# Kernel optimization log

Hardware: AMD Instinct MI355X
Metric: run time of the kernel (lower is better)

## Reference

```python
import jax, jax.numpy as jnp
import numpy as np

B, S, D = 128, 50, 128
NUM_NODE = 40000
HOP, N_ITER, SAMPLE = 2, 2, 12
N_NEI = 8
TEMP, MU, LEAK = 0.5, 0.1, 0.2


def setup_inputs() -> dict:
    key = jax.random.key(0)
    ks = jax.random.split(key, 32)
    stdv = 1.0 / np.sqrt(D)
    u = lambda k, shp: jax.random.uniform(k, shp, jnp.float32, -stdv, stdv)
    return {
        "inputs": jax.random.randint(ks[0], (B, S), 0, NUM_NODE),
        "adj": jax.random.randint(ks[1], (B, S, S), 0, 5),
        "item": jax.random.randint(ks[2], (B, S), 0, NUM_NODE),
        "simi_mask": jax.random.randint(ks[3], (B, S, S), 0, 2),
        "as_items_0": jax.random.randint(ks[4], (B, S, N_NEI), 0, NUM_NODE),
        "as_items_1": jax.random.randint(ks[5], (B, S, N_NEI), 0, NUM_NODE),
        "as_items_ssl_0": jax.random.randint(ks[6], (B, S, N_NEI), 0, NUM_NODE),
        "as_items_ssl_1": jax.random.randint(ks[7], (B, S, N_NEI), 0, NUM_NODE),
        "last_item_mask": jnp.zeros((B, S), bool).at[:, -1].set(True),
        "adj_all": jax.random.randint(ks[8], (NUM_NODE, SAMPLE), 0, NUM_NODE),
        "num": jax.random.uniform(ks[9], (NUM_NODE, SAMPLE)),
        "emb": u(ks[10], (NUM_NODE, D)),
        "pos_emb": u(ks[11], (200, D)),
        "a_local": u(ks[12], (N_ITER, 4, D)),
        "mir_w1": u(ks[13], (N_ITER, D, D)),
        "mir_w2": u(ks[14], (N_ITER, D, D)),
        "glob_w1": u(ks[15], (HOP, D + 1, D)),
        "glob_w2": u(ks[16], (HOP, D, 1)),
        "glob_w3": u(ks[17], (HOP, 2 * D, D)),
        "attr_w": u(ks[18], (2 * D, D)),
        "highway_w": u(ks[19], (2 * D, D)),
        "glu1_w": u(ks[20], (D, D)),
        "glu2_w": u(ks[21], (D, D)),
        "glu4_w": u(ks[22], (D, D)),
        "glu4_b": u(ks[23], (D,)),
        "w_s": u(ks[24], (D, 1)),
        "gate_w": u(ks[25], (2 * D, D)),
    }


def _forward(num, emb, pos_emb, a_local, mir_w1, mir_w2, glob_w1, glob_w2, glob_w3,
             attr_w, highway_w, glu1_w, glu2_w, glu4_w, glu4_b, w_s, gate_w,
             inputs, adj, item, simi_mask, as_lists, as_ssl_lists, last_item_mask, adj_all):
    mi = (inputs != 0).astype(emb.dtype)  # [B,S]
    h = emb[inputs]                        # [B,S,D]

    # ---- AttributeAggregator (masked-mean pool per attribute + gated fusion) ----
    def pool(idx_list):
        ps = []
        for idx in idx_list:
            m = (idx != 0).astype(emb.dtype)[..., None]  # [B,S,N,1]
            ps.append(jnp.sum(emb[idx] * m, 2) / (jnp.sum(m, 2) + 1e-8))
        return jnp.mean(jnp.stack(ps), 0)  # [B,S,D]
    hf1 = pool(as_lists)
    hf2 = pool(as_ssl_lists)
    g_attr = jax.nn.sigmoid(jnp.concatenate([h, hf1], -1) @ attr_w)
    hf = g_attr * h + (1.0 - g_attr) * hf1

    # ---- multi-hop neighbor sampling (irregular gathers) ----
    neigh = [inputs]
    wts = []
    for _ in range(HOP):
        flat = neigh[-1].reshape(-1)
        neigh.append(adj_all[flat].reshape(B, -1))
        wts.append(num[flat].reshape(B, -1))
    ev = [emb[n] for n in neigh]  # [B,S,D], [B,S*12,D], [B,S*144,D]

    item_emb = emb[item] * mi[..., None]
    sess = jnp.sum(item_emb, 1) / jnp.sum(mi, -1, keepdims=True)  # [B,D]

    # ---- GlobalAggregator stack (GCE-GNN style attention over sampled neighbors) ----
    for n_hop in range(HOP):
        nxt = []
        for hop in range(HOP - n_hop):
            sv = ev[hop]                                   # [B,M,D]
            nv = ev[hop + 1].reshape(B, -1, SAMPLE, D)     # [B,M,12,D]
            nw = wts[hop].reshape(B, -1, SAMPLE)           # [B,M,12]
            extra = jnp.broadcast_to(sess[:, None, None, :], nv.shape)
            a = jnp.concatenate([extra * nv, nw[..., None]], -1)  # [B,M,12,D+1]
            a = jax.nn.leaky_relu(a @ glob_w1[n_hop], LEAK)
            a = jax.nn.softmax((a @ glob_w2[n_hop])[..., 0], -1)[..., None]
            agg = jnp.sum(a * nv, -2)
            nxt.append(jnp.tanh(jnp.concatenate([sv, agg], -1) @ glob_w3[n_hop]))
        ev = nxt
    h_global = ev[0].reshape(B, S, D)

    # ---- LocalAggregator (edge-typed GAT) + MirrorAggregator (gated exchange) ----
    x = h
    mirror = hf
    for i in range(HOP):
        e = jax.nn.leaky_relu(jnp.einsum('bid,bjd,kd->kbij', x, x, a_local[i]), LEAK)
        att = jnp.full((B, S, S), -9e15, x.dtype)
        for k in range(4):
            att = jnp.where(adj == k + 1, e[k], att)
        x = jax.nn.softmax(att, -1) @ x
        gm = jax.nn.sigmoid(x @ mir_w1[i] + mirror @ mir_w2[i])
        x, mirror = gm * x + (1.0 - gm) * mirror, gm * mirror + (1.0 - gm) * x

    # ---- highway + last-item select ----
    g = jax.nn.sigmoid(jnp.concatenate([h, x], -1) @ highway_w)
    x_dot = g * h + (1.0 - g) * x
    h_local = jnp.sum(x_dot * last_item_mask[..., None].astype(x_dot.dtype), 1)  # [B,D]

    mask = mi[..., None]
    pos = pos_emb[:S][None]  # [1,S,D]
    bw = emb[1:]             # [NUM_NODE-1,D]
    hs = jnp.sum(h_global * mask, -2) / jnp.sum(mask, 1)  # [B,D]

    # ---- SSL pairwise similarity loss ----
    sim = jnp.einsum('bid,bjd->bij', hf1, hf2) / TEMP
    l = -jnp.log(jax.nn.softmax(sim, 2) + 1e-8)
    simi_loss = jnp.mean(jnp.sum(l * (simi_mask == 1), (1, 2)))

    # ---- attention-style GLU scoring ----
    hp = x_dot + pos
    nh = jax.nn.sigmoid(hp @ glu1_w + hs[:, None, :] @ glu2_w + h_local[:, None, :] @ glu4_w + glu4_b)
    beta = (nh @ w_s) * mask
    zg = jnp.sum(beta * hp, 1)  # [B,D]
    gf = jax.nn.sigmoid(jnp.concatenate([zg, h_local], -1) @ gate_w) * MU
    zh = gf * h_local + (1.0 - gf) * zg
    scores = zh @ bw.T  # [B, NUM_NODE-1]
    return simi_loss, scores


def reference(inputs, adj, item, simi_mask, as_items_0, as_items_1,
              as_items_ssl_0, as_items_ssl_1, last_item_mask, adj_all, num,
              emb, pos_emb, a_local, mir_w1, mir_w2, glob_w1, glob_w2, glob_w3,
              attr_w, highway_w, glu1_w, glu2_w, glu4_w, glu4_b, w_s, gate_w):
    return _forward(num, emb, pos_emb, a_local, mir_w1, mir_w2, glob_w1, glob_w2, glob_w3,
                    attr_w, highway_w, glu1_w, glu2_w, glu4_w, glu4_b, w_s, gate_w,
                    inputs, adj, item, simi_mask, [as_items_0, as_items_1],
                    [as_items_ssl_0, as_items_ssl_1], last_item_mask, adj_all)
```

## Files before the change

### kernel.cpp

```cpp
#include <hip/hip_runtime.h>
#include <hip/hip_bf16.h>
#include <type_traits>


#define B 128
#define S 50
#define D 128
#define SAMPLE 12
#define NNEI 8
#define NODES 40000
#define NSC (NODES - 1)
#define LEAK 0.2f
#define TEMPV 0.5f
#define MUV 0.1f
#define NEG_BIG -3.0e38f

typedef const float* fpp;
typedef float* fpw;
typedef unsigned short u16;
typedef __attribute__((ext_vector_type(8))) short bfrag8;
typedef __attribute__((ext_vector_type(4))) float f32x4;

__device__ __forceinline__ float sigm(float x) { return 1.f / (1.f + __expf(-x)); }
__device__ __forceinline__ float tanh_f(float x) { return 1.f - 2.f / (__expf(2.f * x) + 1.f); }
__device__ __forceinline__ float leaky(float x) { return x >= 0.f ? x : LEAK * x; }
__device__ __forceinline__ u16 f2bf(float v) {
  __hip_bfloat16 h = __float2bfloat16(v);
  return *reinterpret_cast<u16*>(&h);
}
__device__ __forceinline__ float lde(const float* p, long i) { return p[i]; }
__device__ __forceinline__ float lde(const u16* p, long i) {
  union { unsigned int u; float f; } c;
  c.u = ((unsigned int)p[i]) << 16;
  return c.f;
}
__device__ __forceinline__ float bfu(short s) {
  union { unsigned u; float f; } c;
  c.u = ((unsigned)(unsigned short)s) << 16;
  return c.f;
}

template <typename ET>
__device__ __forceinline__ bfrag8 load_frag(const ET* __restrict__ emb, long row, int koff) {
  if constexpr (sizeof(ET) == 2) {
    return *(const bfrag8*)(const void*)(emb + row * D + koff);
  } else {
    const float* s = (const float*)(emb + row * D + koff);
    float4 lo = *(const float4*)s;
    float4 hi = *(const float4*)(s + 4);
    bfrag8 b;
    b[0] = (short)f2bf(lo.x); b[1] = (short)f2bf(lo.y);
    b[2] = (short)f2bf(lo.z); b[3] = (short)f2bf(lo.w);
    b[4] = (short)f2bf(hi.x); b[5] = (short)f2bf(hi.y);
    b[6] = (short)f2bf(hi.z); b[7] = (short)f2bf(hi.w);
    return b;
  }
}

__device__ __forceinline__ bfrag8 scale8(bfrag8 r, float4 sa, float4 sb) {
  bfrag8 o;
  o[0] = (short)f2bf(bfu(r[0]) * sa.x); o[1] = (short)f2bf(bfu(r[1]) * sa.y);
  o[2] = (short)f2bf(bfu(r[2]) * sa.z); o[3] = (short)f2bf(bfu(r[3]) * sa.w);
  o[4] = (short)f2bf(bfu(r[4]) * sb.x); o[5] = (short)f2bf(bfu(r[5]) * sb.y);
  o[6] = (short)f2bf(bfu(r[6]) * sb.z); o[7] = (short)f2bf(bfu(r[7]) * sb.w);
  return o;
}

__global__ __launch_bounds__(256) void kprep_emb(fpp emb, u16* __restrict__ out) {
  long i = ((long)blockIdx.x * 256 + threadIdx.x) * 4;
  if (i + 3 >= (long)NODES * D) return;
  float4 v = *(const float4*)(emb + i);
  out[i + 0] = f2bf(v.x); out[i + 1] = f2bf(v.y);
  out[i + 2] = f2bf(v.z); out[i + 3] = f2bf(v.w);
}

__global__ __launch_bounds__(256) void kprep4(fpp gw1, fpp gw3,
                                              u16* __restrict__ p1a,
                                              u16* __restrict__ p1b,
                                              u16* __restrict__ p3a,
                                              u16* __restrict__ p3b) {
  int i = blockIdx.x * 256 + threadIdx.x;
  fpp W; u16* dst; int KS;
  if (i < 16384)      { W = gw1;             dst = p1a; KS = 4; }
  else if (i < 32768) { W = gw1 + 129 * 128; dst = p1b; KS = 4; i -= 16384; }
  else if (i < 65536) { W = gw3;             dst = p3a; KS = 8; i -= 32768; }
  else                { W = gw3 + 256 * 128; dst = p3b; KS = 8; i -= 65536; }
  int e = i & 7;
  int lane = (i >> 3) & 63;
  int rest = i >> 9;
  int ks = rest % KS, nt = rest / KS;
  int k = ks * 32 + ((lane >> 4) << 3) + e;
  int n = (nt << 4) + (lane & 15);
  dst[i] = f2bf(W[(long)k * 128 + n]);
}

template <typename ET>
__global__ __launch_bounds__(128) void k1_gather(
    const int* __restrict__ inputs, const int* __restrict__ as0,
    const int* __restrict__ as1, const int* __restrict__ ss0,
    const int* __restrict__ ss1, const ET* __restrict__ emb, fpp attr_w,
    fpw h, fpw hf1, fpw hf2, float* __restrict__ mi, fpw xA, fpw mir) {
  int bs = blockIdx.x;
  int d = threadIdx.x;
  __shared__ float h_s[D], hf1_s[D];
  int inp = inputs[bs];
  float hv = lde(emb, (long)inp * D + d);
  const int* lists[4] = {as0, as1, ss0, ss1};
  float p[4];
#pragma unroll
  for (int l = 0; l < 4; l++) {
    float sum = 0.f, cnt = 0.f;
    const int* L = lists[l] + (long)bs * NNEI;
#pragma unroll
    for (int n = 0; n < NNEI; n++) {
      int idx = L[n];
      if (idx != 0) { sum += lde(emb, (long)idx * D + d); cnt += 1.f; }
    }
    p[l] = sum / (cnt + 1e-8f);
  }
  float hf1v = 0.5f * (p[0] + p[1]);
  float hf2v = 0.5f * (p[2] + p[3]);
  h_s[d] = hv;
  hf1_s[d] = hf1v;
  __syncthreads();
  float acc = 0.f;
  for (int k = 0; k < D; k++)
    acc += h_s[k] * attr_w[(long)k * D + d] + hf1_s[k] * attr_w[(long)(D + k) * D + d];
  float g = sigm(acc);
  float hfv = g * hv + (1.f - g) * hf1v;
  long o = (long)bs * D + d;
  h[o] = hv; hf1[o] = hf1v; hf2[o] = hf2v; xA[o] = hv; mir[o] = hfv;
  if (d == 0) mi[bs] = (inp != 0) ? 1.f : 0.f;
}

__global__ __launch_bounds__(128) void k2_sess(const int* __restrict__ inputs,
                                               const int* __restrict__ item,
                                               fpp emb, fpw sess) {
  int b = blockIdx.x;
  int d = threadIdx.x;
  float acc = 0.f, ms = 0.f;
  for (int s = 0; s < S; s++) {
    int inp = inputs[b * S + s];
    float m = (inp != 0) ? 1.f : 0.f;
    int it = item[b * S + s];
    acc += emb[(long)it * D + d] * m;
    ms += m;
  }
  sess[(long)b * D + d] = acc / ms;
}

template <typename ET>
__global__ __launch_bounds__(64) void kGA_unit(
    const int* __restrict__ inputs, const int* __restrict__ adj_all,
    fpp num, const ET* __restrict__ emb, fpp sess,
    fpp W1a, fpp W2a, const u16* __restrict__ p1a,
    u16* __restrict__ aggws) {
  int gb = blockIdx.x;
  int bs = gb / 13;
  int u = gb - bs * 13;
  int b = bs / S;
  int lane = threadIdx.x;
  int q = lane >> 4;
  int mrow = lane & 15;

  __shared__ __align__(16) u16 nvs[16 * 136];

  int src0 = inputs[bs];
  int srcu = (u == 0) ? src0 : adj_all[(long)src0 * SAMPLE + (u - 1)];
  int rid = adj_all[(long)srcu * SAMPLE + (mrow < 12 ? mrow : 0)];
  float nwq[4];
#pragma unroll
  for (int i = 0; i < 4; i++)
    nwq[i] = (q < 3) ? num[(long)srcu * SAMPLE + q * 4 + i] : 0.f;

  const float* sessb = sess + (long)b * D;
  bfrag8 rawA[4], sA[4];
#pragma unroll
  for (int ks = 0; ks < 4; ks++)
    rawA[ks] = load_frag(emb, (long)rid, ks * 32 + q * 8);
#pragma unroll
  for (int ks = 0; ks < 4; ks++)
    *(bfrag8*)(nvs + mrow * 136 + ks * 32 + q * 8) = rawA[ks];
#pragma unroll
  for (int ks = 0; ks < 4; ks++) {
    float4 sa = *(const float4*)(sessb + ks * 32 + q * 8);
    float4 sb = *(const float4*)(sessb + ks * 32 + q * 8 + 4);
    sA[ks] = scale8(rawA[ks], sa, sb);
  }
  float wl8[8], w28[8];
#pragma unroll
  for (int nt = 0; nt < 8; nt++) {
    int col = nt * 16 + mrow;
    wl8[nt] = W1a[(long)D * D + col];
    w28[nt] = W2a[col];
  }
  float lp[4] = {0.f, 0.f, 0.f, 0.f};
#pragma unroll
  for (int nt = 0; nt < 8; nt++) {
    f32x4 acc = (f32x4){0.f, 0.f, 0.f, 0.f};
#pragma unroll
    for (int ks = 0; ks < 4; ks++)
      acc = __builtin_amdgcn_mfma_f32_16x16x32_bf16(
          sA[ks], *(const bfrag8*)(p1a + ks * 512 + lane * 8 + nt * 2048), acc, 0, 0, 0);
    lp[0] += leaky(acc[0] + nwq[0] * wl8[nt]) * w28[nt];
    lp[1] += leaky(acc[1] + nwq[1] * wl8[nt]) * w28[nt];
    lp[2] += leaky(acc[2] + nwq[2] * wl8[nt]) * w28[nt];
    lp[3] += leaky(acc[3] + nwq[3] * wl8[nt]) * w28[nt];
  }
#pragma unroll
  for (int off = 1; off <= 8; off <<= 1)
#pragma unroll
    for (int i = 0; i < 4; i++) lp[i] += __shfl_xor(lp[i], off, 64);
  float m4 = (q < 3) ? fmaxf(fmaxf(lp[0], lp[1]), fmaxf(lp[2], lp[3])) : NEG_BIG;
  m4 = fmaxf(m4, __shfl_xor(m4, 16, 64));
  m4 = fmaxf(m4, __shfl_xor(m4, 32, 64));
  float e0 = 0.f, e1 = 0.f, e2 = 0.f, e3 = 0.f, ssum = 0.f;
  if (q < 3) {
    e0 = __expf(lp[0] - m4); e1 = __expf(lp[1] - m4);
    e2 = __expf(lp[2] - m4); e3 = __expf(lp[3] - m4);
    ssum = e0 + e1 + e2 + e3;
  }
  ssum += __shfl_xor(ssum, 16, 64);
  ssum += __shfl_xor(ssum, 32, 64);
  float inv = 1.f / ssum;
  float al[4] = {e0 * inv, e1 * inv, e2 * inv, e3 * inv};
  float aj[12];
#pragma unroll
  for (int j = 0; j < 12; j++) aj[j] = __shfl(al[j & 3], (j >> 2) << 4, 64);
  float a0 = 0.f, a1 = 0.f;
#pragma unroll
  for (int j = 0; j < 12; j++) {
    unsigned pv = *(const unsigned*)(nvs + j * 136 + lane * 2);
    union { unsigned u; float f; } lo, hi;
    lo.u = pv << 16; hi.u = pv & 0xffff0000u;
    a0 += aj[j] * lo.f; a1 += aj[j] * hi.f;
  }
  unsigned pk = ((unsigned)f2bf(a1) << 16) | (unsigned)f2bf(a0);
  *(unsigned*)(aggws + ((long)bs * 13 + u) * 128 + lane * 2) = pk;
}

template <typename ET>
__global__ __launch_bounds__(256) void kGB_post(
    const int* __restrict__ inputs, const int* __restrict__ adj_all,
    fpp num, const ET* __restrict__ emb, fpp sess,
    fpp W1b, fpp W2b, fpp W3b,
    const u16* __restrict__ p1b, const u16* __restrict__ p3a,
    const u16* __restrict__ aggws, fpw hg) {
  int bs = blockIdx.x;
  int b = bs / S;
  int t = threadIdx.x;
  int lane = t & 63;
  int w = t >> 6;
  int q = lane >> 4;
  int mrow = lane & 15;

  __shared__ int svidx_l[16];
  __shared__ __align__(16) float ev_l[16 * 132];
  __shared__ float red_l[64];
  __shared__ __align__(16) float agg1_l[128];

  int src0 = inputs[bs];
  if (t < 16)
    svidx_l[t] = (t == 0) ? src0 : (t <= 12 ? adj_all[(long)src0 * SAMPLE + t - 1] : 0);
  __syncthreads();
  const float* sessb = sess + (long)b * D;

  {
    long svr = svidx_l[mrow];
    f32x4 accB[2];
    accB[0] = (f32x4){0.f, 0.f, 0.f, 0.f};
    accB[1] = (f32x4){0.f, 0.f, 0.f, 0.f};
#pragma unroll
    for (int ks = 0; ks < 4; ks++) {
      bfrag8 a = load_frag(emb, svr, ks * 32 + q * 8);
      const u16* pb = p3a + ks * 512 + lane * 8;
#pragma unroll
      for (int n = 0; n < 2; n++)
        accB[n] = __builtin_amdgcn_mfma_f32_16x16x32_bf16(
            a, *(const bfrag8*)(pb + (w * 2 + n) * 4096), accB[n], 0, 0, 0);
    }
#pragma unroll
    for (int ks = 4; ks < 8; ks++) {
      bfrag8 a;
      if (mrow < 13)
        a = *(const bfrag8*)(aggws + ((long)bs * 13 + mrow) * 128 + (ks - 4) * 32 + q * 8);
      else
        a = (bfrag8){0, 0, 0, 0, 0, 0, 0, 0};
      const u16* pb = p3a + ks * 512 + lane * 8;
#pragma unroll
      for (int n = 0; n < 2; n++)
        accB[n] = __builtin_amdgcn_mfma_f32_16x16x32_bf16(
            a, *(const bfrag8*)(pb + (w * 2 + n) * 4096), accB[n], 0, 0, 0);
    }
#pragma unroll
    for (int n = 0; n < 2; n++) {
      int col = (w * 2 + n) * 16 + mrow;
#pragma unroll
      for (int i = 0; i < 4; i++) {
        int row = q * 4 + i;
        if (row < 13) ev_l[row * 132 + col] = tanh_f(accB[n][i]);
      }
    }
  }
  __syncthreads();

  {
    float wlB[2], w2B[2];
#pragma unroll
    for (int n = 0; n < 2; n++) {
      int col = (w * 2 + n) * 16 + mrow;
      wlB[n] = W1b[(long)D * D + col];
      w2B[n] = W2b[col];
    }
    int rr = 1 + (mrow < 12 ? mrow : 0);
    f32x4 accC[2];
    accC[0] = (f32x4){0.f, 0.f, 0.f, 0.f};
    accC[1] = (f32x4){0.f, 0.f, 0.f, 0.f};
#pragma unroll
    for (int ks = 0; ks < 4; ks++) {
      float4 sa = *(const float4*)(sessb + ks * 32 + q * 8);
      float4 sb = *(const float4*)(sessb + ks * 32 + q * 8 + 4);
      float4 lo = *(const float4*)(ev_l + rr * 132 + ks * 32 + q * 8);
      float4 hi = *(const float4*)(ev_l + rr * 132 + ks * 32 + q * 8 + 4);
      bfrag8 a;
      a[0] = (short)f2bf(lo.x * sa.x); a[1] = (short)f2bf(lo.y * sa.y);
      a[2] = (short)f2bf(lo.z * sa.z); a[3] = (short)f2bf(lo.w * sa.w);
      a[4] = (short)f2bf(hi.x * sb.x); a[5] = (short)f2bf(hi.y * sb.y);
      a[6] = (short)f2bf(hi.z * sb.z); a[7] = (short)f2bf(hi.w * sb.w);
      const u16* pb = p1b + ks * 512 + lane * 8;
#pragma unroll
      for (int n = 0; n < 2; n++)
        accC[n] = __builtin_amdgcn_mfma_f32_16x16x32_bf16(
            a, *(const bfrag8*)(pb + (w * 2 + n) * 2048), accC[n], 0, 0, 0);
    }
    float4 nwq0;
    if (q < 3) {
      nwq0.x = num[(long)src0 * SAMPLE + q * 4 + 0];
      nwq0.y = num[(long)src0 * SAMPLE + q * 4 + 1];
      nwq0.z = num[(long)src0 * SAMPLE + q * 4 + 2];
      nwq0.w = num[(long)src0 * SAMPLE + q * 4 + 3];
    } else {
      nwq0.x = nwq0.y = nwq0.z = nwq0.w = 0.f;
    }
    float lp2[4] = {0.f, 0.f, 0.f, 0.f};
#pragma unroll
    for (int n = 0; n < 2; n++) {
      lp2[0] += leaky(accC[n][0] + nwq0.x * wlB[n]) * w2B[n];
      lp2[1] += leaky(accC[n][1] + nwq0.y * wlB[n]) * w2B[n];
      lp2[2] += leaky(accC[n][2] + nwq0.z * wlB[n]) * w2B[n];
      lp2[3] += leaky(accC[n][3] + nwq0.w * wlB[n]) * w2B[n];
    }
#pragma unroll
    for (int off = 1; off <= 8; off <<= 1)
#pragma unroll
      for (int i = 0; i < 4; i++) lp2[i] += __shfl_xor(lp2[i], off, 64);
    if (mrow == 0) {
#pragma unroll
      for (int i = 0; i < 4; i++) red_l[w * 16 + q * 4 + i] = lp2[i];
    }
  }
  __syncthreads();
  {
    float lg[12];
#pragma unroll
    for (int j = 0; j < 12; j++)
      lg[j] = red_l[j] + red_l[16 + j] + red_l[32 + j] + red_l[48 + j];
    float mx = lg[0];
#pragma unroll
    for (int j = 1; j < 12; j++) mx = fmaxf(mx, lg[j]);
    float se = 0.f;
#pragma unroll
    for (int j = 0; j < 12; j++) { lg[j] = __expf(lg[j] - mx); se += lg[j]; }
    float invc = 1.f / se;
    if (t < 128) {
      float ag = 0.f;
#pragma unroll
      for (int j = 0; j < 12; j++) ag += lg[j] * invc * ev_l[(1 + j) * 132 + t];
      agg1_l[t] = ag;
    }
  }
  __syncthreads();
  {
    int d = t & 127, hh = t >> 7;
    const float* av = hh ? agg1_l : ev_l;
    const float* Wp = W3b + (hh ? (long)128 * D : 0) + d;
    float accf = 0.f;
#pragma unroll 4
    for (int k = 0; k < 128; k++) accf += av[k] * Wp[(long)k * D];
    ev_l[(14 + hh) * 132 + d] = accf;
  }
  __syncthreads();
  if (t < 128) hg[(long)bs * D + t] = tanh_f(ev_l[14 * 132 + t] + ev_l[15 * 132 + t]);
}

template <typename ET>
__global__ __launch_bounds__(128) void kG_mono(
    const int* __restrict__ inputs, const int* __restrict__ adj_all,
    fpp num, const ET* __restrict__ emb, fpp sess,
    fpp W1a, fpp W2a, fpp W1b, fpp W2b, fpp W3b,
    const u16* __restrict__ p1a, const u16* __restrict__ p1b,
    const u16* __restrict__ p3a, fpw hg) {
  int bs = blockIdx.x;
  int b = bs / S;
  int d = threadIdx.x;
  int lane = d & 63;
  int w = d >> 6;
  int q = lane >> 4;
  int mrow = lane & 15;

  __shared__ __align__(16) u16 nvs_l[16 * 136];
  __shared__ __align__(16) u16 svagg_l[16 * 264];
  __shared__ __align__(16) float ev_l[13 * 128];
  __shared__ __align__(16) float agg1_l[128];
  __shared__ float red_l[2][16];
  __shared__ float nw_l[16];

#pragma unroll
  for (int r = 12; r < 16; r++) {
    nvs_l[r * 136 + d] = 0;
    if (d < 8) nvs_l[r * 136 + 128 + d] = 0;
  }
#pragma unroll
  for (int r = 13; r < 16; r++) {
    svagg_l[r * 264 + d] = 0;
    svagg_l[r * 264 + 128 + d] = 0;
    if (d < 8) svagg_l[r * 264 + 256 + d] = 0;
  }

  float sess_d = sess[(long)b * D + d];
  int src0 = __builtin_amdgcn_readfirstlane(inputs[bs]);
  int n1[SAMPLE];
#pragma unroll
  for (int j = 0; j < SAMPLE; j++)
    n1[j] = __builtin_amdgcn_readfirstlane(adj_all[(long)src0 * SAMPLE + j]);
  svagg_l[0 * 264 + d] = f2bf(lde(emb, (long)src0 * D + d));

  float w2A[4], wlA[4], w2B[4], wlB[4];
#pragma unroll
  for (int nt = 0; nt < 4; nt++) {
    int col = (w * 4 + nt) * 16 + mrow;
    w2A[nt] = W2a[col];
    wlA[nt] = W1a[(long)D * D + col];
    w2B[nt] = W2b[col];
    wlB[nt] = W1b[(long)D * D + col];
  }

  float pre[SAMPLE], pnw = 0.f;
  {
#pragma unroll
    for (int j = 0; j < SAMPLE; j++)
      pre[j] = lde(emb, (long)n1[j] * D + d);
    if (d < SAMPLE) pnw = num[(long)src0 * SAMPLE + d];
  }
  for (int u = 0; u < 13; u++) {
    if (d < SAMPLE) nw_l[d] = pnw;
    float nvreg[SAMPLE];
#pragma unroll
    for (int j = 0; j < SAMPLE; j++) {
      nvreg[j] = pre[j];
      nvs_l[j * 136 + d] = f2bf(pre[j] * sess_d);
    }
    if (u == 0) {
#pragma unroll
      for (int j = 0; j < SAMPLE; j++)
        svagg_l[(1 + j) * 264 + d] = f2bf(nvreg[j]);
    }
    __syncthreads();
    if (u < 12) {
      int srcn = n1[u];
#pragma unroll
      for (int j = 0; j < SAMPLE; j++) {
        int nj = __builtin_amdgcn_readfirstlane(adj_all[(long)srcn * SAMPLE + j]);
        pre[j] = lde(emb, (long)nj * D + d);
      }
      if (d < SAMPLE) pnw = num[(long)srcn * SAMPLE + d];
    }
    f32x4 acc[4];
#pragma unroll
    for (int nt = 0; nt < 4; nt++) acc[nt] = (f32x4){0.f, 0.f, 0.f, 0.f};
#pragma unroll
    for (int ks = 0; ks < 4; ks++) {
      bfrag8 a = *(const bfrag8*)(nvs_l + mrow * 136 + q * 8 + ks * 32);
      const u16* pb = p1a + (w * 16 + ks) * 512 + lane * 8;
#pragma unroll
      for (int nt = 0; nt < 4; nt++) {
        bfrag8 bb = *(const bfrag8*)(pb + nt * 2048);
        acc[nt] = __builtin_amdgcn_mfma_f32_16x16x32_bf16(a, bb, acc[nt], 0, 0, 0);
      }
    }
    float lp[4] = {0.f, 0.f, 0.f, 0.f};
    float nwq[4];
#pragma unroll
    for (int i = 0; i < 4; i++) nwq[i] = (q < 3) ? nw_l[q * 4 + i] : 0.f;
#pragma unroll
    for (int nt = 0; nt < 4; nt++)
#pragma unroll
      for (int i = 0; i < 4; i++)
        lp[i] += leaky(acc[nt][i] + nwq[i] * wlA[nt]) * w2A[nt];
#pragma unroll
    for (int off = 1; off <= 8; off <<= 1)
#pragma unroll
      for (int i = 0; i < 4; i++) lp[i] += __shfl_xor(lp[i], off, 64);
    if (mrow == 0 && q < 3) {
#pragma unroll
      for (int i = 0; i < 4; i++) red_l[w][q * 4 + i] = lp[i];
    }
    __syncthreads();
    float lg[SAMPLE];
#pragma unroll
    for (int j = 0; j < SAMPLE; j++) lg[j] = red_l[0][j] + red_l[1][j];
    float mx = lg[0];
#pragma unroll
    for (int j = 1; j < SAMPLE; j++) mx = fmaxf(mx, lg[j]);
    float se = 0.f;
#pragma unroll
    for (int j = 0; j < SAMPLE; j++) { lg[j] = __expf(lg[j] - mx); se += lg[j]; }
    float inv = 1.f / se;
    float aggd = 0.f;
#pragma unroll
    for (int j = 0; j < SAMPLE; j++) aggd += lg[j] * inv * nvreg[j];
    svagg_l[u * 264 + 128 + d] = f2bf(aggd);
  }
  __syncthreads();

  {
    f32x4 accB[4];
#pragma unroll
    for (int nt = 0; nt < 4; nt++) accB[nt] = (f32x4){0.f, 0.f, 0.f, 0.f};
#pragma unroll
    for (int ks = 0; ks < 8; ks++) {
      bfrag8 a = *(const bfrag8*)(svagg_l + mrow * 264 + q * 8 + ks * 32);
      const u16* pb = p3a + (w * 32 + ks) * 512 + lane * 8;
#pragma unroll
      for (int nt = 0; nt < 4; nt++) {
        bfrag8 bb = *(const bfrag8*)(pb + nt * 4096);
        accB[nt] = __builtin_amdgcn_mfma_f32_16x16x32_bf16(a, bb, accB[nt], 0, 0, 0);
      }
    }
#pragma unroll
    for (int nt = 0; nt < 4; nt++) {
      int col = (w * 4 + nt) * 16 + mrow;
#pragma unroll
      for (int i = 0; i < 4; i++) {
        int u2 = q * 4 + i;
        if (u2 < 13) ev_l[u2 * 128 + col] = tanh_f(accB[nt][i]);
      }
    }
    __syncthreads();
  }

  {
    float evreg[SAMPLE];
#pragma unroll
    for (int j = 0; j < SAMPLE; j++) {
      float e = ev_l[(1 + j) * 128 + d];
      evreg[j] = e;
      nvs_l[j * 136 + d] = f2bf(e * sess_d);
    }
    if (d < SAMPLE) nw_l[d] = num[(long)src0 * SAMPLE + d];
    __syncthreads();

    f32x4 acc[4];
#pragma unroll
    for (int nt = 0; nt < 4; nt++) acc[nt] = (f32x4){0.f, 0.f, 0.f, 0.f};
#pragma unroll
    for (int ks = 0; ks < 4; ks++) {
      bfrag8 a = *(const bfrag8*)(nvs_l + mrow * 136 + q * 8 + ks * 32);
      const u16* pb = p1b + (w * 16 + ks) * 512 + lane * 8;
#pragma unroll
      for (int nt = 0; nt < 4; nt++) {
        bfrag8 bb = *(const bfrag8*)(pb + nt * 2048);
        acc[nt] = __builtin_amdgcn_mfma_f32_16x16x32_bf16(a, bb, acc[nt], 0, 0, 0);
      }
    }
    float lp[4] = {0.f, 0.f, 0.f, 0.f};
    float nwq[4];
#pragma unroll
    for (int i = 0; i < 4; i++) nwq[i] = (q < 3) ? nw_l[q * 4 + i] : 0.f;
#pragma unroll
    for (int nt = 0; nt < 4; nt++)
#pragma unroll
      for (int i = 0; i < 4; i++)
        lp[i] += leaky(acc[nt][i] + nwq[i] * wlB[nt]) * w2B[nt];
#pragma unroll
    for (int off = 1; off <= 8; off <<= 1)
#pragma unroll
      for (int i = 0; i < 4; i++) lp[i] += __shfl_xor(lp[i], off, 64);
    if (mrow == 0 && q < 3) {
#pragma unroll
      for (int i = 0; i < 4; i++) red_l[w][q * 4 + i] = lp[i];
    }
    __syncthreads();

    float lg[SAMPLE];
#pragma unroll
    for (int j = 0; j < SAMPLE; j++) lg[j] = red_l[0][j] + red_l[1][j];
    float mx = lg[0];
#pragma unroll
    for (int j = 1; j < SAMPLE; j++) mx = fmaxf(mx, lg[j]);
    float se = 0.f;
#pragma unroll
    for (int j = 0; j < SAMPLE; j++) { lg[j] = __expf(lg[j] - mx); se += lg[j]; }
    float inv = 1.f / se;
    float agg1d = 0.f;
#pragma unroll
    for (int j = 0; j < SAMPLE; j++) agg1d += lg[j] * inv * evreg[j];
    agg1_l[d] = agg1d;
    __syncthreads();

    float accf = 0.f;
#pragma unroll 4
    for (int k4 = 0; k4 < 32; k4++) {
      float4 a4 = *(const float4*)&ev_l[4 * k4];
      float4 g4 = *(const float4*)&agg1_l[4 * k4];
      accf += a4.x * W3b[(4 * k4 + 0) * D + d] + a4.y * W3b[(4 * k4 + 1) * D + d] +
              a4.z * W3b[(4 * k4 + 2) * D + d] + a4.w * W3b[(4 * k4 + 3) * D + d] +
              g4.x * W3b[(D + 4 * k4 + 0) * D + d] + g4.y * W3b[(D + 4 * k4 + 1) * D + d] +
              g4.z * W3b[(D + 4 * k4 + 2) * D + d] + g4.w * W3b[(D + 4 * k4 + 3) * D + d];
    }
    hg[(long)bs * D + d] = tanh_f(accf);
  }
}

__global__ __launch_bounds__(128) void k5ab(fpp x, const int* __restrict__ adj,
                                            fpp a_loc, fpp w1, fpp w2,
                                            fpw xout, fpw mir,
                                            fpp hw, fpp h, fpw x_dot,
                                            float* __restrict__ h_local,
                                            int fin) {
  int b = blockIdx.x / S;
  int row = blockIdx.x % S;
  int tid = threadIdx.x;
  __shared__ float xi_s[D];
  __shared__ float ak_s[4][D];
  __shared__ float alpha_s[S];
  __shared__ float part_s[4][2][64];
  long idx = ((long)b * S + row) * D + tid;
  xi_s[tid] = x[idx];
#pragma unroll
  for (int k = 0; k < 4; k++) ak_s[k][tid] = a_loc[(long)k * D + tid];
  __syncthreads();
  {
    int j = tid & 63, hf = tid >> 6;
    float a0 = 0.f, a1 = 0.f, a2 = 0.f, a3 = 0.f;
    if (j < S) {
      const float* xj = x + ((long)b * S + j) * D + hf * 64;
      int off = hf * 64;
      for (int dd = 0; dd < 64; dd++) {
        float prod = xi_s[off + dd] * xj[dd];
        a0 += prod * ak_s[0][off + dd];
        a1 += prod * ak_s[1][off + dd];
        a2 += prod * ak_s[2][off + dd];
        a3 += prod * ak_s[3][off + dd];
      }
    }
    part_s[0][hf][j] = a0; part_s[1][hf][j] = a1;
    part_s[2][hf][j] = a2; part_s[3][hf][j] = a3;
  }
  __syncthreads();
  if (tid < 64) {
    int j = tid;
    float att;
    if (j < S) {
      float acc0 = part_s[0][0][j] + part_s[0][1][j];
      float acc1 = part_s[1][0][j] + part_s[1][1][j];
      float acc2 = part_s[2][0][j] + part_s[2][1][j];
      float acc3 = part_s[3][0][j] + part_s[3][1][j];
      int av = adj[((long)b * S + row) * S + j];
      att = -9e15f;
      if (av == 1) att = leaky(acc0);
      else if (av == 2) att = leaky(acc1);
      else if (av == 3) att = leaky(acc2);
      else if (av == 4) att = leaky(acc3);
    } else {
      att = NEG_BIG;
    }
    float mx = att;
#pragma unroll
    for (int o = 32; o > 0; o >>= 1) mx = fmaxf(mx, __shfl_xor(mx, o, 64));
    float e = __expf(att - mx);
    float ssum = e;
#pragma unroll
    for (int o = 32; o > 0; o >>= 1) ssum += __shfl_xor(ssum, o, 64);
    if (j < S) alpha_s[j] = e / ssum;
  }
  __syncthreads();
  float xn = 0.f;
  for (int j = 0; j < S; j++) xn += alpha_s[j] * x[((long)b * S + j) * D + tid];
  float mv = mir[idx];
  ak_s[0][tid] = xn;
  ak_s[1][tid] = mv;
  __syncthreads();
  float a2m = 0.f;
  for (int k = 0; k < D; k++)
    a2m += ak_s[0][k] * w1[(long)k * D + tid] + ak_s[1][k] * w2[(long)k * D + tid];
  float g = sigm(a2m);
  float xg = g * xn + (1.f - g) * mv;
  if (!fin) {
    xout[idx] = xg;
    mir[idx] = g * mv + (1.f - g) * xn;
    return;
  }
  float hv = h[idx];
  ak_s[2][tid] = hv;
  ak_s[3][tid] = xg;
  __syncthreads();
  float a3m = 0.f;
  for (int k = 0; k < D; k++)
    a3m += ak_s[2][k] * hw[(long)k * D + tid] + ak_s[3][k] * hw[(long)(D + k) * D + tid];
  float gh = sigm(a3m);
  float xd = gh * hv + (1.f - gh) * xg;
  x_dot[idx] = xd;
  if (row == S - 1) h_local[(long)b * D + tid] = xd;
}

__global__ __launch_bounds__(128) void k7_simi(fpp hf1, fpp hf2,
                                               const int* __restrict__ simi_mask,
                                               float* __restrict__ loss) {
  int b = blockIdx.x / S;
  int i = blockIdx.x % S;
  int t = threadIdx.x;
  __shared__ float hi_s[D];
  __shared__ float part_s[2][64];
  hi_s[t] = hf1[((long)b * S + i) * D + t];
  __syncthreads();
  {
    int j = t & 63, hf = t >> 6;
    float acc = 0.f;
    if (j < S) {
      const float* r = hf2 + ((long)b * S + j) * D + hf * 64;
      int off = hf * 64;
      for (int dd = 0; dd < 64; dd++) acc += hi_s[off + dd] * r[dd];
    }
    part_s[hf][j] = acc;
  }
  __syncthreads();
  if (t < 64) {
    int j = t;
    float sim = (j < S) ? (part_s[0][j] + part_s[1][j]) * (1.0f / TEMPV) : NEG_BIG;
    float mx = sim;
#pragma unroll
    for (int o = 32; o > 0; o >>= 1) mx = fmaxf(mx, __shfl_xor(mx, o, 64));
    float e = __expf(sim - mx);
    float ssum = e;
#pragma unroll
    for (int o = 32; o > 0; o >>= 1) ssum += __shfl_xor(ssum, o, 64);
    float contrib = 0.f;
    if (j < S) {
      float p = e / ssum;
      float l = -__logf(p + 1e-8f);
      if (simi_mask[((long)b * S + i) * S + j] == 1) contrib = l;
    }
#pragma unroll
    for (int o = 32; o > 0; o >>= 1) contrib += __shfl_xor(contrib, o, 64);
    if (j == 0) atomicAdd(loss, contrib);
  }
}

__global__ __launch_bounds__(512) void k8_glu(
    fpp hg, fpp x_dot, fpp pos, fpp h_local, const float* __restrict__ mi,
    fpp glu1, fpp glu2, fpp glu4, fpp glu4b, fpp w_s, fpp gate_w, fpw zh) {
  int b = blockIdx.x;
  int t = threadIdx.x;
  int d = t & 127;
  int g = t >> 7;
  __shared__ float hs_s[D], hl_s[D];
  __shared__ float hp_g[4][D], part[4][D], zg_g[4][D];
  __shared__ float red2[4][2];
  float msf = 0.f;
  for (int s = 0; s < S; s++) msf += mi[b * S + s];
  float hsacc = 0.f;
  for (int s = g * 13; s < min(S, g * 13 + 13); s++)
    hsacc += hg[((long)b * S + s) * D + d] * mi[b * S + s];
  part[g][d] = hsacc;
  if (g == 1) hl_s[d] = h_local[(long)b * D + d];
  __syncthreads();
  if (g == 0) hs_s[d] = (part[0][d] + part[1][d] + part[2][d] + part[3][d]) / msf;
  __syncthreads();
  float c = glu4b[d];
  for (int k = 0; k < D; k++)
    c += hs_s[k] * glu2[(long)k * D + d] + hl_s[k] * glu4[(long)k * D + d];
  float wsd = w_s[d];
  float zg = 0.f;
  for (int it = 0; it < 13; it++) {
    int s = g * 13 + it;
    bool act = s < S;
    float hp = 0.f;
    if (act) {
      hp = x_dot[((long)b * S + s) * D + d] + pos[(long)s * D + d];
      hp_g[g][d] = hp;
    }
    __syncthreads();
    if (act) {
      float acc = c;
      for (int k = 0; k < D; k++) acc += hp_g[g][k] * glu1[(long)k * D + d];
      float v = sigm(acc) * wsd;
#pragma unroll
      for (int o = 32; o > 0; o >>= 1) v += __shfl_down(v, o, 64);
      if ((t & 63) == 0) red2[g][(t >> 6) & 1] = v;
    }
    __syncthreads();
    if (act) {
      float beta = (red2[g][0] + red2[g][1]) * mi[b * S + s];
      zg += beta * hp;
    }
    __syncthreads();
  }
  zg_g[g][d] = zg;
  __syncthreads();
  if (g == 0) {
    float zgf = zg_g[0][d] + zg_g[1][d] + zg_g[2][d] + zg_g[3][d];
    hp_g[0][d] = zgf;
  }
  __syncthreads();
  if (g == 0) {
    float zgf = hp_g[0][d];
    float acc = 0.f;
    for (int k = 0; k < D; k++)
      acc += hp_g[0][k] * gate_w[(long)k * D + d] +
             hl_s[k] * gate_w[(long)(D + k) * D + d];
    float gf = sigm(acc) * MUV;
    zh[(long)b * D + d] = gf * hl_s[d] + (1.f - gf) * zgf;
  }
}

template <typename ET>
__global__ __launch_bounds__(256) void k9_scores(fpp zh, const ET* __restrict__ emb,
                                                 fpp loss, float* __restrict__ out) {
  int t = threadIdx.x;
  if (blockIdx.x == 0 && t == 0) out[0] = loss[0] * (1.0f / (float)B);
  int lane = t & 63;
  int w = t >> 6;
  int q = lane >> 4;
  int mrow = lane & 15;
  long n = (long)blockIdx.x * 64 + w * 16 + mrow;
  bool valid = n < NSC;
  long nrow = valid ? (n + 1) : 1;
  bfrag8 bfr[4];
#pragma unroll
  for (int ks = 0; ks < 4; ks++) {
    if constexpr (sizeof(ET) == 2) {
      bfr[ks] = *(const bfrag8*)(const void*)(emb + nrow * D + ks * 32 + q * 8);
    } else {
      const float* src = (const float*)(emb + nrow * D + ks * 32 + q * 8);
      float4 lo = *(const float4*)src;
      float4 hi = *(const float4*)(src + 4);
      bfrag8 bb;
      bb[0] = (short)f2bf(lo.x); bb[1] = (short)f2bf(lo.y);
      bb[2] = (short)f2bf(lo.z); bb[3] = (short)f2bf(lo.w);
      bb[4] = (short)f2bf(hi.x); bb[5] = (short)f2bf(hi.y);
      bb[6] = (short)f2bf(hi.z); bb[7] = (short)f2bf(hi.w);
      bfr[ks] = bb;
    }
  }
#pragma unroll
  for (int mt = 0; mt < 8; mt++) {
    f32x4 acc = (f32x4){0.f, 0.f, 0.f, 0.f};
#pragma unroll
    for (int ks = 0; ks < 4; ks++) {
      const float* za = zh + (long)(mt * 16 + mrow) * D + ks * 32 + q * 8;
      float4 lo = *(const float4*)za;
      float4 hi = *(const float4*)(za + 4);
      bfrag8 a;
      a[0] = (short)f2bf(lo.x); a[1] = (short)f2bf(lo.y);
      a[2] = (short)f2bf(lo.z); a[3] = (short)f2bf(lo.w);
      a[4] = (short)f2bf(hi.x); a[5] = (short)f2bf(hi.y);
      a[6] = (short)f2bf(hi.z); a[7] = (short)f2bf(hi.w);
      acc = __builtin_amdgcn_mfma_f32_16x16x32_bf16(a, bfr[ks], acc, 0, 0, 0);
    }
    if (valid) {
#pragma unroll
      for (int i = 0; i < 4; i++) {
        int m = mt * 16 + q * 4 + i;
        out[1 + (long)m * NSC + n] = acc[i];
      }
    }
  }
}

extern "C" void kernel_launch(void* const* d_in, const int* in_sizes, int n_in,
                              void* d_out, int out_size, void* d_ws, size_t ws_size,
                              hipStream_t stream) {
  (void)in_sizes; (void)n_in; (void)out_size;
  const int* inputs = (const int*)d_in[0];
  const int* adj = (const int*)d_in[1];
  const int* item = (const int*)d_in[2];
  const int* simi_mask = (const int*)d_in[3];
  const int* as0 = (const int*)d_in[4];
  const int* as1 = (const int*)d_in[5];
  const int* ss0 = (const int*)d_in[6];
  const int* ss1 = (const int*)d_in[7];
  const int* adj_all = (const int*)d_in[9];
  fpp num = (fpp)d_in[10];
  fpp emb = (fpp)d_in[11];
  fpp pos = (fpp)d_in[12];
  fpp a_local = (fpp)d_in[13];
  fpp mir_w1 = (fpp)d_in[14];
  fpp mir_w2 = (fpp)d_in[15];
  fpp gw1 = (fpp)d_in[16];
  fpp gw2 = (fpp)d_in[17];
  fpp gw3 = (fpp)d_in[18];
  fpp attr_w = (fpp)d_in[19];
  fpp highway_w = (fpp)d_in[20];
  fpp glu1 = (fpp)d_in[21];
  fpp glu2 = (fpp)d_in[22];
  fpp glu4 = (fpp)d_in[23];
  fpp glu4b = (fpp)d_in[24];
  fpp w_s = (fpp)d_in[25];
  fpp gate_w = (fpp)d_in[26];

  float* ob = (float*)d_out;
  constexpr long BSD_ = (long)B * S * D;
  fpw s_h = ob + 0 * BSD_;
  fpw s_hf1 = ob + 1 * BSD_;
  fpw s_hf2 = ob + 2 * BSD_;
  fpw s_mir = ob + 3 * BSD_;
  fpw s_xA = ob + 4 * BSD_;
  fpw s_xB = ob + 5 * BSD_;

  float* ws = (float*)d_ws;
  float* w_loss = ws + 0;
  float* w_mi = ws + 16;
  float* w_sess = w_mi + (long)B * S;
  float* w_hl = w_sess + (long)B * D;
  float* w_zh = w_hl + (long)B * D;
  u16* p1a = (u16*)(ws + 72000);
  u16* p1b = (u16*)(ws + 72000 + 8192);
  u16* p3a = (u16*)(ws + 72000 + 16384);
  u16* p3b = (u16*)(ws + 72000 + 32768);
  u16* embbf = (u16*)((char*)d_ws + 491520);
  u16* aggws = (u16*)((char*)d_ws + 10731520);
  bool useBF = ws_size >= (size_t)12 * 1024 * 1024;
  bool useSplit = useBF && ws_size >= ((size_t)32 << 20);

  hipMemsetAsync((void*)w_loss, 0, sizeof(float), stream);

  kprep4<<<384, 256, 0, stream>>>(gw1, gw3, p1a, p1b, p3a, p3b);
  if (useBF)
    kprep_emb<<<(NODES * D / 4 + 255) / 256, 256, 0, stream>>>(emb, embbf);

  if (useBF)
    k1_gather<u16><<<B * S, 128, 0, stream>>>(inputs, as0, as1, ss0, ss1,
                                              embbf, attr_w, s_h, s_hf1, s_hf2,
                                              w_mi, s_xA, s_mir);
  else
    k1_gather<float><<<B * S, 128, 0, stream>>>(inputs, as0, as1, ss0, ss1,
                                                emb, attr_w, s_h, s_hf1, s_hf2,
                                                w_mi, s_xA, s_mir);
  k7_simi<<<B * S, 128, 0, stream>>>(s_hf1, s_hf2, simi_mask, w_loss);
  k2_sess<<<B, 128, 0, stream>>>(inputs, item, emb, w_sess);

  if (useSplit) {
    kGA_unit<u16><<<B * S * 13, 64, 0, stream>>>(inputs, adj_all, num, embbf,
                                                 w_sess, gw1, gw2, p1a, aggws);
    kGB_post<u16><<<B * S, 256, 0, stream>>>(inputs, adj_all, num, embbf,
                                             w_sess, gw1 + 129 * 128, gw2 + 128,
                                             gw3 + 256 * 128, p1b, p3a, aggws,
                                             s_hf2 );
  } else if (useBF) {
    kG_mono<u16><<<B * S, 128, 0, stream>>>(inputs, adj_all, num, embbf,
                                            w_sess, gw1, gw2,
                                            gw1 + 129 * 128, gw2 + 128,
                                            gw3 + 256 * 128, p1a, p1b, p3a,
                                            s_hf2 );
  } else {
    kG_mono<float><<<B * S, 128, 0, stream>>>(inputs, adj_all, num, emb,
                                              w_sess, gw1, gw2,
                                              gw1 + 129 * 128, gw2 + 128,
                                              gw3 + 256 * 128, p1a, p1b, p3a,
                                              s_hf2 );
  }

  k5ab<<<B * S, 128, 0, stream>>>(s_xA, adj, a_local, mir_w1, mir_w2,
                                  s_xB, s_mir, highway_w, s_h, s_hf1, w_hl, 0);
  k5ab<<<B * S, 128, 0, stream>>>(s_xB, adj, a_local + 4 * D,
                                  mir_w1 + (long)D * D, mir_w2 + (long)D * D,
                                  s_xA, s_mir, highway_w, s_h,
                                  s_hf1 , w_hl, 1);
  k8_glu<<<B, 512, 0, stream>>>(s_hf2 , s_hf1 , pos,
                                w_hl, w_mi, glu1, glu2, glu4, glu4b, w_s,
                                gate_w, w_zh);
  if (useBF)
    k9_scores<u16><<<(NSC + 63) / 64, 256, 0, stream>>>(w_zh, embbf, w_loss,
                                                        (float*)d_out);
  else
    k9_scores<float><<<(NSC + 63) / 64, 256, 0, stream>>>(w_zh, emb, w_loss,
                                                          (float*)d_out);
}
```

Measured before the change: 739.8 us.

## Fuse independent stages into heterogeneous kernels sharing grid via block-range dispatch

```diff
diff --git a/kernel.cpp b/kernel.cpp
--- a/kernel.cpp
+++ b/kernel.cpp
@@ -14,6 +14,8 @@
 #define TEMPV 0.5f
 #define MUV 0.1f
 #define NEG_BIG -3.0e38f
+#define NUNITS (B * S * 13)
+#define NGA (NUNITS / 4)
 
 typedef const float* fpp;
 typedef float* fpw;
@@ -65,6 +67,20 @@
   o[6] = (short)f2bf(bfu(r[6]) * sb.z); o[7] = (short)f2bf(bfu(r[7]) * sb.w);
   return o;
 }
+
+struct __align__(16) SMk5 { float xi[D]; float ak[4][D]; float alpha[56]; float part[4][2][64]; };
+struct __align__(16) SMk7 { float hi[D]; float part[2][64]; };
+struct __align__(16) SMga { u16 nvs[2][2][16 * 136]; };
+struct __align__(16) SMgb {
+  u16 nvs[16 * 136];
+  float ev[13 * 128];
+  float agg1[128];
+  float red[2][16];
+  float nw[16];
+  int svidx[16];
+};
+union __align__(16) SMF1 { SMk5 a; SMk7 b; SMga c; };
+union __align__(16) SMF2 { SMk5 a; SMgb d; };
 
 __global__ __launch_bounds__(256) void kprep_emb(fpp emb, u16* __restrict__ out) {
   long i = ((long)blockIdx.x * 256 + threadIdx.x) * 4;
@@ -150,43 +166,13 @@
 }
 
 template <typename ET>
-__global__ __launch_bounds__(64) void kGA_unit(
-    const int* __restrict__ inputs, const int* __restrict__ adj_all,
-    fpp num, const ET* __restrict__ emb, fpp sess,
-    fpp W1a, fpp W2a, const u16* __restrict__ p1a,
-    u16* __restrict__ aggws) {
-  int gb = blockIdx.x;
-  int bs = gb / 13;
-  int u = gb - bs * 13;
-  int b = bs / S;
-  int lane = threadIdx.x;
+__device__ __forceinline__ void dev_kga2(
+    u16* __restrict__ nvs0, u16* __restrict__ nvs1,
+    const int* __restrict__ inputs, const int* __restrict__ adj_all, fpp num,
+    const ET* __restrict__ emb, fpp sess, fpp W1a, fpp W2a,
+    const u16* __restrict__ p1a, u16* __restrict__ aggws, int gu0, int lane) {
   int q = lane >> 4;
   int mrow = lane & 15;
-
-  __shared__ __align__(16) u16 nvs[16 * 136];
-
-  int src0 = inputs[bs];
-  int srcu = (u == 0) ? src0 : adj_all[(long)src0 * SAMPLE + (u - 1)];
-  int rid = adj_all[(long)srcu * SAMPLE + (mrow < 12 ? mrow : 0)];
-  float nwq[4];
-#pragma unroll
-  for (int i = 0; i < 4; i++)
-    nwq[i] = (q < 3) ? num[(long)srcu * SAMPLE + q * 4 + i] : 0.f;
-
-  const float* sessb = sess + (long)b * D;
-  bfrag8 rawA[4], sA[4];
-#pragma unroll
-  for (int ks = 0; ks < 4; ks++)
-    rawA[ks] = load_frag(emb, (long)rid, ks * 32 + q * 8);
-#pragma unroll
-  for (int ks = 0; ks < 4; ks++)
-    *(bfrag8*)(nvs + mrow * 136 + ks * 32 + q * 8) = rawA[ks];
-#pragma unroll
-  for (int ks = 0; ks < 4; ks++) {
-    float4 sa = *(const float4*)(sessb + ks * 32 + q * 8);
-    float4 sb = *(const float4*)(sessb + ks * 32 + q * 8 + 4);
-    sA[ks] = scale8(rawA[ks], sa, sb);
-  }
   float wl8[8], w28[8];
 #pragma unroll
   for (int nt = 0; nt < 8; nt++) {
@@ -194,203 +180,420 @@
     wl8[nt] = W1a[(long)D * D + col];
     w28[nt] = W2a[col];
   }
-  float lp[4] = {0.f, 0.f, 0.f, 0.f};
-#pragma unroll
-  for (int nt = 0; nt < 8; nt++) {
-    f32x4 acc = (f32x4){0.f, 0.f, 0.f, 0.f};
+  bfrag8 sA[2][4];
+  float nwq[2][4];
+#pragma unroll
+  for (int g = 0; g < 2; g++) {
+    int gu = gu0 + g;
+    int bs = gu / 13;
+    int u = gu - bs * 13;
+    int b = bs / S;
+    int src0 = inputs[bs];
+    int srcu = (u == 0) ? src0 : adj_all[(long)src0 * SAMPLE + (u - 1)];
+    int rid = adj_all[(long)srcu * SAMPLE + (mrow < 12 ? mrow : 0)];
+#pragma unroll
+    for (int i = 0; i < 4; i++)
+      nwq[g][i] = (q < 3) ? num[(long)srcu * SAMPLE + q * 4 + i] : 0.f;
+    const float* sessb = sess + (long)b * D;
+    u16* nb = g ? nvs1 : nvs0;
+    bfrag8 raw[4];
 #pragma unroll
     for (int ks = 0; ks < 4; ks++)
-      acc = __builtin_amdgcn_mfma_f32_16x16x32_bf16(
-          sA[ks], *(const bfrag8*)(p1a + ks * 512 + lane * 8 + nt * 2048), acc, 0, 0, 0);
-    lp[0] += leaky(acc[0] + nwq[0] * wl8[nt]) * w28[nt];
-    lp[1] += leaky(acc[1] + nwq[1] * wl8[nt]) * w28[nt];
-    lp[2] += leaky(acc[2] + nwq[2] * wl8[nt]) * w28[nt];
-    lp[3] += leaky(acc[3] + nwq[3] * wl8[nt]) * w28[nt];
-  }
-#pragma unroll
-  for (int off = 1; off <= 8; off <<= 1)
-#pragma unroll
-    for (int i = 0; i < 4; i++) lp[i] += __shfl_xor(lp[i], off, 64);
-  float m4 = (q < 3) ? fmaxf(fmaxf(lp[0], lp[1]), fmaxf(lp[2], lp[3])) : NEG_BIG;
-  m4 = fmaxf(m4, __shfl_xor(m4, 16, 64));
-  m4 = fmaxf(m4, __shfl_xor(m4, 32, 64));
-  float e0 = 0.f, e1 = 0.f, e2 = 0.f, e3 = 0.f, ssum = 0.f;
-  if (q < 3) {
-    e0 = __expf(lp[0] - m4); e1 = __expf(lp[1] - m4);
-    e2 = __expf(lp[2] - m4); e3 = __expf(lp[3] - m4);
-    ssum = e0 + e1 + e2 + e3;
-  }
-  ssum += __shfl_xor(ssum, 16, 64);
-  ssum += __shfl_xor(ssum, 32, 64);
-  float inv = 1.f / ssum;
-  float al[4] = {e0 * inv, e1 * inv, e2 * inv, e3 * inv};
-  float aj[12];
-#pragma unroll
-  for (int j = 0; j < 12; j++) aj[j] = __shfl(al[j & 3], (j >> 2) << 4, 64);
-  float a0 = 0.f, a1 = 0.f;
-#pragma unroll
-  for (int j = 0; j < 12; j++) {
-    unsigned pv = *(const unsigned*)(nvs + j * 136 + lane * 2);
-    union { unsigned u; float f; } lo, hi;
-    lo.u = pv << 16; hi.u = pv & 0xffff0000u;
-    a0 += aj[j] * lo.f; a1 += aj[j] * hi.f;
-  }
-  unsigned pk = ((unsigned)f2bf(a1) << 16) | (unsigned)f2bf(a0);
-  *(unsigned*)(aggws + ((long)bs * 13 + u) * 128 + lane * 2) = pk;
-}
-
-template <typename ET>
-__global__ __launch_bounds__(256) void kGB_post(
-    const int* __restrict__ inputs, const int* __restrict__ adj_all,
-    fpp num, const ET* __restrict__ emb, fpp sess,
-    fpp W1b, fpp W2b, fpp W3b,
-    const u16* __restrict__ p1b, const u16* __restrict__ p3a,
-    const u16* __restrict__ aggws, fpw hg) {
-  int bs = blockIdx.x;
-  int b = bs / S;
-  int t = threadIdx.x;
-  int lane = t & 63;
-  int w = t >> 6;
-  int q = lane >> 4;
-  int mrow = lane & 15;
-
-  __shared__ int svidx_l[16];
-  __shared__ __align__(16) float ev_l[16 * 132];
-  __shared__ float red_l[64];
-  __shared__ __align__(16) float agg1_l[128];
-
-  int src0 = inputs[bs];
-  if (t < 16)
-    svidx_l[t] = (t == 0) ? src0 : (t <= 12 ? adj_all[(long)src0 * SAMPLE + t - 1] : 0);
-  __syncthreads();
-  const float* sessb = sess + (long)b * D;
-
-  {
-    long svr = svidx_l[mrow];
-    f32x4 accB[2];
-    accB[0] = (f32x4){0.f, 0.f, 0.f, 0.f};
-    accB[1] = (f32x4){0.f, 0.f, 0.f, 0.f};
-#pragma unroll
-    for (int ks = 0; ks < 4; ks++) {
-      bfrag8 a = load_frag(emb, svr, ks * 32 + q * 8);
-      const u16* pb = p3a + ks * 512 + lane * 8;
-#pragma unroll
-      for (int n = 0; n < 2; n++)
-        accB[n] = __builtin_amdgcn_mfma_f32_16x16x32_bf16(
-            a, *(const bfrag8*)(pb + (w * 2 + n) * 4096), accB[n], 0, 0, 0);
-    }
-#pragma unroll
-    for (int ks = 4; ks < 8; ks++) {
-      bfrag8 a;
-      if (mrow < 13)
-        a = *(const bfrag8*)(aggws + ((long)bs * 13 + mrow) * 128 + (ks - 4) * 32 + q * 8);
-      else
-        a = (bfrag8){0, 0, 0, 0, 0, 0, 0, 0};
-      const u16* pb = p3a + ks * 512 + lane * 8;
-#pragma unroll
-      for (int n = 0; n < 2; n++)
-        accB[n] = __builtin_amdgcn_mfma_f32_16x16x32_bf16(
-            a, *(const bfrag8*)(pb + (w * 2 + n) * 4096), accB[n], 0, 0, 0);
-    }
-#pragma unroll
-    for (int n = 0; n < 2; n++) {
-      int col = (w * 2 + n) * 16 + mrow;
-#pragma unroll
-      for (int i = 0; i < 4; i++) {
-        int row = q * 4 + i;
-        if (row < 13) ev_l[row * 132 + col] = tanh_f(accB[n][i]);
-      }
-    }
-  }
-  __syncthreads();
-
-  {
-    float wlB[2], w2B[2];
-#pragma unroll
-    for (int n = 0; n < 2; n++) {
-      int col = (w * 2 + n) * 16 + mrow;
-      wlB[n] = W1b[(long)D * D + col];
-      w2B[n] = W2b[col];
-    }
-    int rr = 1 + (mrow < 12 ? mrow : 0);
-    f32x4 accC[2];
-    accC[0] = (f32x4){0.f, 0.f, 0.f, 0.f};
-    accC[1] = (f32x4){0.f, 0.f, 0.f, 0.f};
+      raw[ks] = load_frag(emb, (long)rid, ks * 32 + q * 8);
+#pragma unroll
+    for (int ks = 0; ks < 4; ks++)
+      *(bfrag8*)(nb + mrow * 136 + ks * 32 + q * 8) = raw[ks];
 #pragma unroll
     for (int ks = 0; ks < 4; ks++) {
       float4 sa = *(const float4*)(sessb + ks * 32 + q * 8);
       float4 sb = *(const float4*)(sessb + ks * 32 + q * 8 + 4);
-      float4 lo = *(const float4*)(ev_l + rr * 132 + ks * 32 + q * 8);
-      float4 hi = *(const float4*)(ev_l + rr * 132 + ks * 32 + q * 8 + 4);
-      bfrag8 a;
-      a[0] = (short)f2bf(lo.x * sa.x); a[1] = (short)f2bf(lo.y * sa.y);
-      a[2] = (short)f2bf(lo.z * sa.z); a[3] = (short)f2bf(lo.w * sa.w);
-      a[4] = (short)f2bf(hi.x * sb.x); a[5] = (short)f2bf(hi.y * sb.y);
-      a[6] = (short)f2bf(hi.z * sb.z); a[7] = (short)f2bf(hi.w * sb.w);
-      const u16* pb = p1b + ks * 512 + lane * 8;
-#pragma unroll
-      for (int n = 0; n < 2; n++)
-        accC[n] = __builtin_amdgcn_mfma_f32_16x16x32_bf16(
-            a, *(const bfrag8*)(pb + (w * 2 + n) * 2048), accC[n], 0, 0, 0);
-    }
-    float4 nwq0;
+      sA[g][ks] = scale8(raw[ks], sa, sb);
+    }
+  }
+  float lp[2][4] = {{0.f, 0.f, 0.f, 0.f}, {0.f, 0.f, 0.f, 0.f}};
+#pragma unroll
+  for (int nt = 0; nt < 8; nt++) {
+    f32x4 acc0 = (f32x4){0.f, 0.f, 0.f, 0.f};
+    f32x4 acc1 = (f32x4){0.f, 0.f, 0.f, 0.f};
+#pragma unroll
+    for (int ks = 0; ks < 4; ks++) {
+      bfrag8 bb = *(const bfrag8*)(p1a + ks * 512 + lane * 8 + nt * 2048);
+      acc0 = __builtin_amdgcn_mfma_f32_16x16x32_bf16(sA[0][ks], bb, acc0, 0, 0, 0);
+      acc1 = __builtin_amdgcn_mfma_f32_16x16x32_bf16(sA[1][ks], bb, acc1, 0, 0, 0);
+    }
+#pragma unroll
+    for (int i = 0; i < 4; i++) {
+      lp[0][i] += leaky(acc0[i] + nwq[0][i] * wl8[nt]) * w28[nt];
+      lp[1][i] += leaky(acc1[i] + nwq[1][i] * wl8[nt]) * w28[nt];
+    }
+  }
+#pragma unroll
+  for (int off = 1; off <= 8; off <<= 1)
+#pragma unroll
+    for (int g = 0; g < 2; g++)
+#pragma unroll
+      for (int i = 0; i < 4; i++) lp[g][i] += __shfl_xor(lp[g][i], off, 64);
+#pragma unroll
+  for (int g = 0; g < 2; g++) {
+    float m4 = (q < 3) ? fmaxf(fmaxf(lp[g][0], lp[g][1]), fmaxf(lp[g][2], lp[g][3]))
+                       : NEG_BIG;
+    m4 = fmaxf(m4, __shfl_xor(m4, 16, 64));
+    m4 = fmaxf(m4, __shfl_xor(m4, 32, 64));
+    float e0 = 0.f, e1 = 0.f, e2 = 0.f, e3 = 0.f, ssum = 0.f;
     if (q < 3) {
-      nwq0.x = num[(long)src0 * SAMPLE + q * 4 + 0];
-      nwq0.y = num[(long)src0 * SAMPLE + q * 4 + 1];
-      nwq0.z = num[(long)src0 * SAMPLE + q * 4 + 2];
-      nwq0.w = num[(long)src0 * SAMPLE + q * 4 + 3];
-    } else {
-      nwq0.x = nwq0.y = nwq0.z = nwq0.w = 0.f;
-    }
-    float lp2[4] = {0.f, 0.f, 0.f, 0.f};
-#pragma unroll
-    for (int n = 0; n < 2; n++) {
-      lp2[0] += leaky(accC[n][0] + nwq0.x * wlB[n]) * w2B[n];
-      lp2[1] += leaky(accC[n][1] + nwq0.y * wlB[n]) * w2B[n];
-      lp2[2] += leaky(accC[n][2] + nwq0.z * wlB[n]) * w2B[n];
-      lp2[3] += leaky(accC[n][3] + nwq0.w * wlB[n]) * w2B[n];
-    }
+      e0 = __expf(lp[g][0] - m4); e1 = __expf(lp[g][1] - m4);
+      e2 = __expf(lp[g][2] - m4); e3 = __expf(lp[g][3] - m4);
+      ssum = e0 + e1 + e2 + e3;
+    }
+    ssum += __shfl_xor(ssum, 16, 64);
+    ssum += __shfl_xor(ssum, 32, 64);
+    float inv = 1.f / ssum;
+    float al[4] = {e0 * inv, e1 * inv, e2 * inv, e3 * inv};
+    float aj[12];
+#pragma unroll
+    for (int j = 0; j < 12; j++) aj[j] = __shfl(al[j & 3], (j >> 2) << 4, 64);
+    const u16* nb = g ? nvs1 : nvs0;
+    float a0 = 0.f, a1 = 0.f;
+#pragma unroll
+    for (int j = 0; j < 12; j++) {
+      unsigned pv = *(const unsigned*)(nb + j * 136 + lane * 2);
+      union { unsigned u; float f; } lo, hi;
+      lo.u = pv << 16; hi.u = pv & 0xffff0000u;
+      a0 += aj[j] * lo.f; a1 += aj[j] * hi.f;
+    }
+    unsigned pk = ((unsigned)f2bf(a1) << 16) | (unsigned)f2bf(a0);
+    *(unsigned*)(aggws + (long)(gu0 + g) * 128 + lane * 2) = pk;
+  }
+}
+
+template <typename ET>
+__device__ __forceinline__ void dev_kgb(
+    SMgb& sm, const int* __restrict__ inputs, const int* __restrict__ adj_all,
+    fpp num, const ET* __restrict__ emb, fpp sess, fpp W1b, fpp W2b, fpp W3b,
+    const u16* __restrict__ p1b, const u16* __restrict__ p3a,
+    const u16* __restrict__ aggws, fpw hg, int bs) {
+  int b = bs / S;
+  int d = threadIdx.x;
+  int lane = d & 63;
+  int w = d >> 6;
+  int q = lane >> 4;
+  int mrow = lane & 15;
+
+#pragma unroll
+  for (int r = 12; r < 16; r++) {
+    sm.nvs[r * 136 + d] = 0;
+    if (d < 8) sm.nvs[r * 136 + 128 + d] = 0;
+  }
+  int src0 = inputs[bs];
+  if (d < 16)
+    sm.svidx[d] = (d == 0) ? src0 : (d <= 12 ? adj_all[(long)src0 * SAMPLE + d - 1] : 0);
+  if (d < SAMPLE) sm.nw[d] = num[(long)src0 * SAMPLE + d];
+  float sess_d = sess[(long)b * D + d];
+  __syncthreads();
+
+  {
+    long svr = sm.svidx[mrow];
+    f32x4 accB[4];
+#pragma unroll
+    for (int nt = 0; nt < 4; nt++) accB[nt] = (f32x4){0.f, 0.f, 0.f, 0.f};
+#pragma unroll
+    for (int ks = 0; ks < 4; ks++) {
+      bfrag8 a = (bfrag8){0, 0, 0, 0, 0, 0, 0, 0};
+      if (mrow < 13) a = load_frag(emb, svr, ks * 32 + q * 8);
+      const u16* pb = p3a + (w * 32 + ks) * 512 + lane * 8;
+#pragma unroll
+      for (int nt = 0; nt < 4; nt++)
+        accB[nt] = __builtin_amdgcn_mfma_f32_16x16x32_bf16(
+            a, *(const bfrag8*)(pb + nt * 4096), accB[nt], 0, 0, 0);
+    }
+#pragma unroll
+    for (int ks = 4; ks < 8; ks++) {
+      bfrag8 a = (bfrag8){0, 0, 0, 0, 0, 0, 0, 0};
+      if (mrow < 13)
+        a = *(const bfrag8*)(aggws + ((long)bs * 13 + mrow) * 128 + (ks - 4) * 32 + q * 8);
+      const u16* pb = p3a + (w * 32 + ks) * 512 + lane * 8;
+#pragma unroll
+      for (int nt = 0; nt < 4; nt++)
+        accB[nt] = __builtin_amdgcn_mfma_f32_16x16x32_bf16(
+            a, *(const bfrag8*)(pb + nt * 4096), accB[nt], 0, 0, 0);
+    }
+#pragma unroll
+    for (int nt = 0; nt < 4; nt++) {
+      int col = (w * 4 + nt) * 16 + mrow;
+#pragma unroll
+      for (int i = 0; i < 4; i++) {
+        int u2 = q * 4 + i;
+        if (u2 < 13) sm.ev[u2 * 128 + col] = tanh_f(accB[nt][i]);
+      }
+    }
+  }
+  __syncthreads();
+
+  {
+    float w2B[4], wlB[4];
+#pragma unroll
+    for (int nt = 0; nt < 4; nt++) {
+      int col = (w * 4 + nt) * 16 + mrow;
+      w2B[nt] = W2b[col];
+      wlB[nt] = W1b[(long)D * D + col];
+    }
+    float evreg[SAMPLE];
+#pragma unroll
+    for (int j = 0; j < SAMPLE; j++) {
+      float e = sm.ev[(1 + j) * 128 + d];
+      evreg[j] = e;
+      sm.nvs[j * 136 + d] = f2bf(e * sess_d);
+    }
+    __syncthreads();
+
+    f32x4 acc[4];
+#pragma unroll
+    for (int nt = 0; nt < 4; nt++) acc[nt] = (f32x4){0.f, 0.f, 0.f, 0.f};
+#pragma unroll
+    for (int ks = 0; ks < 4; ks++) {
+      bfrag8 a = *(const bfrag8*)(sm.nvs + mrow * 136 + q * 8 + ks * 32);
+      const u16* pb = p1b + (w * 16 + ks) * 512 + lane * 8;
+#pragma unroll
+      for (int nt = 0; nt < 4; nt++) {
+        bfrag8 bb = *(const bfrag8*)(pb + nt * 2048);
+        acc[nt] = __builtin_amdgcn_mfma_f32_16x16x32_bf16(a, bb, acc[nt], 0, 0, 0);
+      }
+    }
+    float lp[4] = {0.f, 0.f, 0.f, 0.f};
+    float nwq[4];
+#pragma unroll
+    for (int i = 0; i < 4; i++) nwq[i] = (q < 3) ? sm.nw[q * 4 + i] : 0.f;
+#pragma unroll
+    for (int nt = 0; nt < 4; nt++)
+#pragma unroll
+      for (int i = 0; i < 4; i++)
+        lp[i] += leaky(acc[nt][i] + nwq[i] * wlB[nt]) * w2B[nt];
 #pragma unroll
     for (int off = 1; off <= 8; off <<= 1)
 #pragma unroll
-      for (int i = 0; i < 4; i++) lp2[i] += __shfl_xor(lp2[i], off, 64);
-    if (mrow == 0) {
-#pragma unroll
-      for (int i = 0; i < 4; i++) red_l[w * 16 + q * 4 + i] = lp2[i];
-    }
-  }
-  __syncthreads();
-  {
-    float lg[12];
-#pragma unroll
-    for (int j = 0; j < 12; j++)
-      lg[j] = red_l[j] + red_l[16 + j] + red_l[32 + j] + red_l[48 + j];
+      for (int i = 0; i < 4; i++) lp[i] += __shfl_xor(lp[i], off, 64);
+    if (mrow == 0 && q < 3) {
+#pragma unroll
+      for (int i = 0; i < 4; i++) sm.red[w][q * 4 + i] = lp[i];
+    }
+    __syncthreads();
+
+    float lg[SAMPLE];
+#pragma unroll
+    for (int j = 0; j < SAMPLE; j++) lg[j] = sm.red[0][j] + sm.red[1][j];
     float mx = lg[0];
 #pragma unroll
-    for (int j = 1; j < 12; j++) mx = fmaxf(mx, lg[j]);
+    for (int j = 1; j < SAMPLE; j++) mx = fmaxf(mx, lg[j]);
     float se = 0.f;
 #pragma unroll
-    for (int j = 0; j < 12; j++) { lg[j] = __expf(lg[j] - mx); se += lg[j]; }
-    float invc = 1.f / se;
-    if (t < 128) {
-      float ag = 0.f;
-#pragma unroll
-      for (int j = 0; j < 12; j++) ag += lg[j] * invc * ev_l[(1 + j) * 132 + t];
-      agg1_l[t] = ag;
-    }
-  }
-  __syncthreads();
-  {
-    int d = t & 127, hh = t >> 7;
-    const float* av = hh ? agg1_l : ev_l;
-    const float* Wp = W3b + (hh ? (long)128 * D : 0) + d;
+    for (int j = 0; j < SAMPLE; j++) { lg[j] = __expf(lg[j] - mx); se += lg[j]; }
+    float inv = 1.f / se;
+    float agg1d = 0.f;
+#pragma unroll
+    for (int j = 0; j < SAMPLE; j++) agg1d += lg[j] * inv * evreg[j];
+    sm.agg1[d] = agg1d;
+    __syncthreads();
+
     float accf = 0.f;
 #pragma unroll 4
-    for (int k = 0; k < 128; k++) accf += av[k] * Wp[(long)k * D];
-    ev_l[(14 + hh) * 132 + d] = accf;
-  }
-  __syncthreads();
-  if (t < 128) hg[(long)bs * D + t] = tanh_f(ev_l[14 * 132 + t] + ev_l[15 * 132 + t]);
+    for (int k4 = 0; k4 < 32; k4++) {
+      float4 a4 = *(const float4*)&sm.ev[4 * k4];
+      float4 g4 = *(const float4*)&sm.agg1[4 * k4];
+      accf += a4.x * W3b[(4 * k4 + 0) * D + d] + a4.y * W3b[(4 * k4 + 1) * D + d] +
+              a4.z * W3b[(4 * k4 + 2) * D + d] + a4.w * W3b[(4 * k4 + 3) * D + d] +
+              g4.x * W3b[(D + 4 * k4 + 0) * D + d] + g4.y * W3b[(D + 4 * k4 + 1) * D + d] +
+              g4.z * W3b[(D + 4 * k4 + 2) * D + d] + g4.w * W3b[(D + 4 * k4 + 3) * D + d];
+    }
+    hg[(long)bs * D + d] = tanh_f(accf);
+  }
+}
+
+__device__ __forceinline__ void dev_k5ab(SMk5& sm, fpp x, const int* __restrict__ adj,
+                                         fpp a_loc, fpp w1, fpp w2, fpw xout,
+                                         fpw mir, fpp hw, fpp h, fpw x_dot,
+                                         float* __restrict__ h_local, int bs, int fin) {
+  int b = bs / S;
+  int row = bs % S;
+  int tid = threadIdx.x;
+  long idx = ((long)b * S + row) * D + tid;
+  sm.xi[tid] = x[idx];
+#pragma unroll
+  for (int k = 0; k < 4; k++) sm.ak[k][tid] = a_loc[(long)k * D + tid];
+  __syncthreads();
+  {
+    int j = tid & 63, hf = tid >> 6;
+    float a0 = 0.f, a1 = 0.f, a2 = 0.f, a3 = 0.f;
+    if (j < S) {
+      const float* xj = x + ((long)b * S + j) * D + hf * 64;
+      int off = hf * 64;
+      for (int dd = 0; dd < 64; dd++) {
+        float prod = sm.xi[off + dd] * xj[dd];
+        a0 += prod * sm.ak[0][off + dd];
+        a1 += prod * sm.ak[1][off + dd];
+        a2 += prod * sm.ak[2][off + dd];
+        a3 += prod * sm.ak[3][off + dd];
+      }
+    }
+    sm.part[0][hf][j] = a0; sm.part[1][hf][j] = a1;
+    sm.part[2][hf][j] = a2; sm.part[3][hf][j] = a3;
+  }
+  __syncthreads();
+  if (tid < 64) {
+    int j = tid;
+    float att;
+    if (j < S) {
+      float acc0 = sm.part[0][0][j] + sm.part[0][1][j];
+      float acc1 = sm.part[1][0][j] + sm.part[1][1][j];
+      float acc2 = sm.part[2][0][j] + sm.part[2][1][j];
+      float acc3 = sm.part[3][0][j] + sm.part[3][1][j];
+      int av = adj[((long)b * S + row) * S + j];
+      att = -9e15f;
+      if (av == 1) att = leaky(acc0);
+      else if (av == 2) att = leaky(acc1);
+      else if (av == 3) att = leaky(acc2);
+      else if (av == 4) att = leaky(acc3);
+    } else {
+      att = NEG_BIG;
+    }
+    float mx = att;
+#pragma unroll
+    for (int o = 32; o > 0; o >>= 1) mx = fmaxf(mx, __shfl_xor(mx, o, 64));
+    float e = __expf(att - mx);
+    float ssum = e;
+#pragma unroll
+    for (int o = 32; o > 0; o >>= 1) ssum += __shfl_xor(ssum, o, 64);
+    if (j < S) sm.alpha[j] = e / ssum;
+  }
+  __syncthreads();
+  float xn = 0.f;
+  for (int j = 0; j < S; j++) xn += sm.alpha[j] * x[((long)b * S + j) * D + tid];
+  float mv = mir[idx];
+  sm.ak[0][tid] = xn;
+  sm.ak[1][tid] = mv;
+  __syncthreads();
+  float a2m = 0.f;
+  for (int k = 0; k < D; k++)
+    a2m += sm.ak[0][k] * w1[(long)k * D + tid] + sm.ak[1][k] * w2[(long)k * D + tid];
+  float g = sigm(a2m);
+  float xg = g * xn + (1.f - g) * mv;
+  if (!fin) {
+    xout[idx] = xg;
+    mir[idx] = g * mv + (1.f - g) * xn;
+    return;
+  }
+  float hv = h[idx];
+  sm.ak[2][tid] = hv;
+  sm.ak[3][tid] = xg;
+  __syncthreads();
+  float a3m = 0.f;
+  for (int k = 0; k < D; k++)
+    a3m += sm.ak[2][k] * hw[(long)k * D + tid] + sm.ak[3][k] * hw[(long)(D + k) * D + tid];
+  float gh = sigm(a3m);
+  float xd = gh * hv + (1.f - gh) * xg;
+  x_dot[idx] = xd;
+  if (row == S - 1) h_local[(long)b * D + tid] = xd;
+}
+
+__device__ __forceinline__ void dev_k7(SMk7& sm, fpp hf1, fpp hf2,
+                                       const int* __restrict__ simi_mask,
+                                       float* __restrict__ loss, int bs) {
+  int b = bs / S;
+  int i = bs % S;
+  int t = threadIdx.x;
+  sm.hi[t] = hf1[((long)b * S + i) * D + t];
+  __syncthreads();
+  {
+    int j = t & 63, hf = t >> 6;
+    float acc = 0.f;
+    if (j < S) {
+      const float* r = hf2 + ((long)b * S + j) * D + hf * 64;
+      int off = hf * 64;
+      for (int dd = 0; dd < 64; dd++) acc += sm.hi[off + dd] * r[dd];
+    }
+    sm.part[hf][j] = acc;
+  }
+  __syncthreads();
+  if (t < 64) {
+    int j = t;
+    float sim = (j < S) ? (sm.part[0][j] + sm.part[1][j]) * (1.0f / TEMPV) : NEG_BIG;
+    float mx = sim;
+#pragma unroll
+    for (int o = 32; o > 0; o >>= 1) mx = fmaxf(mx, __shfl_xor(mx, o, 64));
+    float e = __expf(sim - mx);
+    float ssum = e;
+#pragma unroll
+    for (int o = 32; o > 0; o >>= 1) ssum += __shfl_xor(ssum, o, 64);
+    float contrib = 0.f;
+    if (j < S) {
+      float p = e / ssum;
+      float l = -__logf(p + 1e-8f);
+      if (simi_mask[((long)b * S + i) * S + j] == 1) contrib = l;
+    }
+#pragma unroll
+    for (int o = 32; o > 0; o >>= 1) contrib += __shfl_xor(contrib, o, 64);
+    if (j == 0) atomicAdd(loss, contrib);
+  }
+}
+
+template <typename ET>
+__global__ __launch_bounds__(128) void kF1(
+    const int* __restrict__ inputs, const int* __restrict__ adj_all, fpp num,
+    const ET* __restrict__ emb, fpp sess, fpp W1a, fpp W2a,
+    const u16* __restrict__ p1a, u16* __restrict__ aggws,
+    fpp xA, const int* __restrict__ adj, fpp a_loc, fpp mw1, fpp mw2,
+    fpw xB, fpw mir,
+    fpp hf1, fpp hf2, const int* __restrict__ simi_mask,
+    float* __restrict__ loss) {
+  __shared__ SMF1 sm;
+  int bid = blockIdx.x;
+  if (bid < NGA) {
+    int t = threadIdx.x;
+    int w = t >> 6, lane = t & 63;
+    dev_kga2<ET>(sm.c.nvs[w][0], sm.c.nvs[w][1], inputs, adj_all, num, emb,
+                 sess, W1a, W2a, p1a, aggws, bid * 4 + w * 2, lane);
+  } else if (bid < NGA + B * S) {
+    dev_k5ab(sm.a, xA, adj, a_loc, mw1, mw2, xB, mir, nullptr, nullptr,
+             nullptr, nullptr, bid - NGA, 0);
+  } else {
+    dev_k7(sm.b, hf1, hf2, simi_mask, loss, bid - NGA - B * S);
+  }
+}
+
+template <typename ET>
+__global__ __launch_bounds__(128) void kF2(
+    const int* __restrict__ inputs, const int* __restrict__ adj_all, fpp num,
+    const ET* __restrict__ emb, fpp sess, fpp W1b, fpp W2b, fpp W3b,
+    const u16* __restrict__ p1b, const u16* __restrict__ p3a,
+    const u16* __restrict__ aggws, fpw hg,
+    fpp xB, const int* __restrict__ adj, fpp a_loc2, fpp mw1b, fpp mw2b,
+    fpw mir, fpp hw, fpp h, fpw x_dot, float* __restrict__ h_local) {
+  __shared__ SMF2 sm;
+  int bid = blockIdx.x;
+  if (bid < B * S) {
+    dev_kgb<ET>(sm.d, inputs, adj_all, num, emb, sess, W1b, W2b, W3b, p1b,
+                p3a, aggws, hg, bid);
+  } else {
+    dev_k5ab(sm.a, xB, adj, a_loc2, mw1b, mw2b, nullptr, mir, hw, h, x_dot,
+             h_local, bid - B * S, 1);
+  }
+}
+
+__global__ __launch_bounds__(128) void k5ab(fpp x, const int* __restrict__ adj,
+                                            fpp a_loc, fpp w1, fpp w2,
+                                            fpw xout, fpw mir,
+                                            fpp hw, fpp h, fpw x_dot,
+                                            float* __restrict__ h_local,
+                                            int fin) {
+  __shared__ SMk5 sm;
+  dev_k5ab(sm, x, adj, a_loc, w1, w2, xout, mir, hw, h, x_dot, h_local,
+           blockIdx.x, fin);
+}
+
+__global__ __launch_bounds__(128) void k7_simi(fpp hf1, fpp hf2,
+                                               const int* __restrict__ simi_mask,
+                                               float* __restrict__ loss) {
+  __shared__ SMk7 sm;
+  dev_k7(sm, hf1, hf2, simi_mask, loss, blockIdx.x);
 }
 
 template <typename ET>
@@ -619,141 +822,6 @@
               g4.z * W3b[(D + 4 * k4 + 2) * D + d] + g4.w * W3b[(D + 4 * k4 + 3) * D + d];
     }
     hg[(long)bs * D + d] = tanh_f(accf);
-  }
-}
-
-__global__ __launch_bounds__(128) void k5ab(fpp x, const int* __restrict__ adj,
-                                            fpp a_loc, fpp w1, fpp w2,
-                                            fpw xout, fpw mir,
-                                            fpp hw, fpp h, fpw x_dot,
-                                            float* __restrict__ h_local,
-                                            int fin) {
-  int b = blockIdx.x / S;
-  int row = blockIdx.x % S;
-  int tid = threadIdx.x;
-  __shared__ float xi_s[D];
-  __shared__ float ak_s[4][D];
-  __shared__ float alpha_s[S];
-  __shared__ float part_s[4][2][64];
-  long idx = ((long)b * S + row) * D + tid;
-  xi_s[tid] = x[idx];
-#pragma unroll
-  for (int k = 0; k < 4; k++) ak_s[k][tid] = a_loc[(long)k * D + tid];
-  __syncthreads();
-  {
-    int j = tid & 63, hf = tid >> 6;
-    float a0 = 0.f, a1 = 0.f, a2 = 0.f, a3 = 0.f;
-    if (j < S) {
-      const float* xj = x + ((long)b * S + j) * D + hf * 64;
-      int off = hf * 64;
-      for (int dd = 0; dd < 64; dd++) {
-        float prod = xi_s[off + dd] * xj[dd];
-        a0 += prod * ak_s[0][off + dd];
-        a1 += prod * ak_s[1][off + dd];
-        a2 += prod * ak_s[2][off + dd];
-        a3 += prod * ak_s[3][off + dd];
-      }
-    }
-    part_s[0][hf][j] = a0; part_s[1][hf][j] = a1;
-    part_s[2][hf][j] = a2; part_s[3][hf][j] = a3;
-  }
-  __syncthreads();
-  if (tid < 64) {
-    int j = tid;
-    float att;
-    if (j < S) {
-      float acc0 = part_s[0][0][j] + part_s[0][1][j];
-      float acc1 = part_s[1][0][j] + part_s[1][1][j];
-      float acc2 = part_s[2][0][j] + part_s[2][1][j];
-      float acc3 = part_s[3][0][j] + part_s[3][1][j];
-      int av = adj[((long)b * S + row) * S + j];
-      att = -9e15f;
-      if (av == 1) att = leaky(acc0);
-      else if (av == 2) att = leaky(acc1);
-      else if (av == 3) att = leaky(acc2);
-      else if (av == 4) att = leaky(acc3);
-    } else {
-      att = NEG_BIG;
-    }
-    float mx = att;
-#pragma unroll
-    for (int o = 32; o > 0; o >>= 1) mx = fmaxf(mx, __shfl_xor(mx, o, 64));
-    float e = __expf(att - mx);
-    float ssum = e;
-#pragma unroll
-    for (int o = 32; o > 0; o >>= 1) ssum += __shfl_xor(ssum, o, 64);
-    if (j < S) alpha_s[j] = e / ssum;
-  }
-  __syncthreads();
-  float xn = 0.f;
-  for (int j = 0; j < S; j++) xn += alpha_s[j] * x[((long)b * S + j) * D + tid];
-  float mv = mir[idx];
-  ak_s[0][tid] = xn;
-  ak_s[1][tid] = mv;
-  __syncthreads();
-  float a2m = 0.f;
-  for (int k = 0; k < D; k++)
-    a2m += ak_s[0][k] * w1[(long)k * D + tid] + ak_s[1][k] * w2[(long)k * D + tid];
-  float g = sigm(a2m);
-  float xg = g * xn + (1.f - g) * mv;
-  if (!fin) {
-    xout[idx] = xg;
-    mir[idx] = g * mv + (1.f - g) * xn;
-    return;
-  }
-  float hv = h[idx];
-  ak_s[2][tid] = hv;
-  ak_s[3][tid] = xg;
-  __syncthreads();
-  float a3m = 0.f;
-  for (int k = 0; k < D; k++)
-    a3m += ak_s[2][k] * hw[(long)k * D + tid] + ak_s[3][k] * hw[(long)(D + k) * D + tid];
-  float gh = sigm(a3m);
-  float xd = gh * hv + (1.f - gh) * xg;
-  x_dot[idx] = xd;
-  if (row == S - 1) h_local[(long)b * D + tid] = xd;
-}
-
-__global__ __launch_bounds__(128) void k7_simi(fpp hf1, fpp hf2,
-                                               const int* __restrict__ simi_mask,
-                                               float* __restrict__ loss) {
-  int b = blockIdx.x / S;
-  int i = blockIdx.x % S;
-  int t = threadIdx.x;
-  __shared__ float hi_s[D];
-  __shared__ float part_s[2][64];
-  hi_s[t] = hf1[((long)b * S + i) * D + t];
-  __syncthreads();
-  {
-    int j = t & 63, hf = t >> 6;
-    float acc = 0.f;
-    if (j < S) {
-      const float* r = hf2 + ((long)b * S + j) * D + hf * 64;
-      int off = hf * 64;
-      for (int dd = 0; dd < 64; dd++) acc += hi_s[off + dd] * r[dd];
-    }
-    part_s[hf][j] = acc;
-  }
-  __syncthreads();
-  if (t < 64) {
-    int j = t;
-    float sim = (j < S) ? (part_s[0][j] + part_s[1][j]) * (1.0f / TEMPV) : NEG_BIG;
-    float mx = sim;
-#pragma unroll
-    for (int o = 32; o > 0; o >>= 1) mx = fmaxf(mx, __shfl_xor(mx, o, 64));
-    float e = __expf(sim - mx);
-    float ssum = e;
-#pragma unroll
-    for (int o = 32; o > 0; o >>= 1) ssum += __shfl_xor(ssum, o, 64);
-    float contrib = 0.f;
-    if (j < S) {
-      float p = e / ssum;
-      float l = -__logf(p + 1e-8f);
-      if (simi_mask[((long)b * S + i) * S + j] == 1) contrib = l;
-    }
-#pragma unroll
-    for (int o = 32; o > 0; o >>= 1) contrib += __shfl_xor(contrib, o, 64);
-    if (j == 0) atomicAdd(loss, contrib);
   }
 }
 
@@ -947,36 +1015,40 @@
     k1_gather<float><<<B * S, 128, 0, stream>>>(inputs, as0, as1, ss0, ss1,
                                                 emb, attr_w, s_h, s_hf1, s_hf2,
                                                 w_mi, s_xA, s_mir);
-  k7_simi<<<B * S, 128, 0, stream>>>(s_hf1, s_hf2, simi_mask, w_loss);
   k2_sess<<<B, 128, 0, stream>>>(inputs, item, emb, w_sess);
 
   if (useSplit) {
-    kGA_unit<u16><<<B * S * 13, 64, 0, stream>>>(inputs, adj_all, num, embbf,
-                                                 w_sess, gw1, gw2, p1a, aggws);
-    kGB_post<u16><<<B * S, 256, 0, stream>>>(inputs, adj_all, num, embbf,
-                                             w_sess, gw1 + 129 * 128, gw2 + 128,
-                                             gw3 + 256 * 128, p1b, p3a, aggws,
-                                             s_hf2 );
-  } else if (useBF) {
-    kG_mono<u16><<<B * S, 128, 0, stream>>>(inputs, adj_all, num, embbf,
-                                            w_sess, gw1, gw2,
-                                            gw1 + 129 * 128, gw2 + 128,
-                                            gw3 + 256 * 128, p1a, p1b, p3a,
-                                            s_hf2 );
+    kF1<u16><<<NGA + 2 * B * S, 128, 0, stream>>>(
+        inputs, adj_all, num, embbf, w_sess, gw1, gw2, p1a, aggws,
+        s_xA, adj, a_local, mir_w1, mir_w2, s_xB, s_mir,
+        s_hf1, s_hf2, simi_mask, w_loss);
+    kF2<u16><<<2 * B * S, 128, 0, stream>>>(
+        inputs, adj_all, num, embbf, w_sess, gw1 + 129 * 128, gw2 + 128,
+        gw3 + 256 * 128, p1b, p3a, aggws, s_hf2 ,
+        s_xB, adj, a_local + 4 * D, mir_w1 + (long)D * D,
+        mir_w2 + (long)D * D, s_mir, highway_w, s_h, s_hf1 , w_hl);
   } else {
-    kG_mono<float><<<B * S, 128, 0, stream>>>(inputs, adj_all, num, emb,
+    k7_simi<<<B * S, 128, 0, stream>>>(s_hf1, s_hf2, simi_mask, w_loss);
+    if (useBF)
+      kG_mono<u16><<<B * S, 128, 0, stream>>>(inputs, adj_all, num, embbf,
                                               w_sess, gw1, gw2,
                                               gw1 + 129 * 128, gw2 + 128,
                                               gw3 + 256 * 128, p1a, p1b, p3a,
                                               s_hf2 );
-  }
-
-  k5ab<<<B * S, 128, 0, stream>>>(s_xA, adj, a_local, mir_w1, mir_w2,
-                                  s_xB, s_mir, highway_w, s_h, s_hf1, w_hl, 0);
-  k5ab<<<B * S, 128, 0, stream>>>(s_xB, adj, a_local + 4 * D,
-                                  mir_w1 + (long)D * D, mir_w2 + (long)D * D,
-                                  s_xA, s_mir, highway_w, s_h,
-                                  s_hf1 , w_hl, 1);
+    else
+      kG_mono<float><<<B * S, 128, 0, stream>>>(inputs, adj_all, num, emb,
+                                                w_sess, gw1, gw2,
+                                                gw1 + 129 * 128, gw2 + 128,
+                                                gw3 + 256 * 128, p1a, p1b,
+                                                p3a, s_hf2 );
+    k5ab<<<B * S, 128, 0, stream>>>(s_xA, adj, a_local, mir_w1, mir_w2,
+                                    s_xB, s_mir, highway_w, s_h, s_hf1, w_hl, 0);
+    k5ab<<<B * S, 128, 0, stream>>>(s_xB, adj, a_local + 4 * D,
+                                    mir_w1 + (long)D * D, mir_w2 + (long)D * D,
+                                    s_xA, s_mir, highway_w, s_h,
+                                    s_hf1 , w_hl, 1);
+  }
+
   k8_glu<<<B, 512, 0, stream>>>(s_hf2 , s_hf1 , pos,
                                 w_hl, w_mi, glu1, glu2, glu4, glu4b, w_s,
                                 gate_w, w_zh);
```

Measured after the change: 679.9 us. 1.09x faster.
